# Kernel tuning notes

Measured on AMD Instinct MI355X. Metric: run time of the kernel, lower is better.

Reference implementation:

```python
import jax, jax.numpy as jnp
import numpy as np

B, T, C, H, D = 4, 2048, 1024, 16, 64
EPS = 1e-5

def setup_inputs() -> dict:
    key = jax.random.key(0)
    ks = jax.random.split(key, 8)
    s = lambda fan_in: 1.0 / np.sqrt(fan_in)
    return {
        'x': jax.random.normal(ks[0], (B, T, C), jnp.float32),
        'wq': jax.random.normal(ks[1], (H, C, D), jnp.float32) * s(C),
        'wk': jax.random.normal(ks[2], (H, C, D), jnp.float32) * s(C),
        'wv': jax.random.normal(ks[3], (H, C, D), jnp.float32) * s(C),
        'w_proj': jax.random.normal(ks[4], (C, C), jnp.float32) * s(C),
        'b_proj': jnp.zeros((C,), jnp.float32),
        'w1': jax.random.normal(ks[5], (C, 4 * C), jnp.float32) * s(C),
        'b1': jnp.zeros((4 * C,), jnp.float32),
        'w2': jax.random.normal(ks[6], (4 * C, C), jnp.float32) * s(4 * C),
        'b2': jnp.zeros((C,), jnp.float32),
        'g1': jnp.ones((C,), jnp.float32),
        'be1': jnp.zeros((C,), jnp.float32),
        'g2': jnp.ones((C,), jnp.float32),
        'be2': jnp.zeros((C,), jnp.float32),
    }

def layer_norm(x, g, b):
    mu = jnp.mean(x, axis=-1, keepdims=True)
    var = jnp.mean(jnp.square(x - mu), axis=-1, keepdims=True)
    return (x - mu) * jax.lax.rsqrt(var + EPS) * g + b

def reference(x, wq, wk, wv, w_proj, b_proj, w1, b1, w2, b2, g1, be1, g2, be2):
    # --- attention (pre-LN) ---
    xn = layer_norm(x, g1, be1)
    q = jnp.einsum('btc,hcd->bhtd', xn, wq)
    k = jnp.einsum('btc,hcd->bhtd', xn, wk)
    v = jnp.einsum('btc,hcd->bhtd', xn, wv)
    # NOTE: original scales by full embedding dim C (not head size)
    scores = jnp.einsum('bhtd,bhsd->bhts', q, k) * (C ** -0.5)
    causal = jnp.tril(jnp.ones((T, T), bool))
    scores = jnp.where(causal, scores, -jnp.inf)
    wei = jax.nn.softmax(scores, axis=-1)
    attn = jnp.einsum('bhts,bhsd->bhtd', wei, v)
    attn = attn.transpose(0, 2, 1, 3).reshape(B, T, C)  # concat heads
    x = x + attn @ w_proj + b_proj
    # --- FFN (pre-LN) ---
    xn2 = layer_norm(x, g2, be2)
    h = jax.nn.relu(xn2 @ w1 + b1)
    x = x + h @ w2 + b2
    return x
```

## Files before the change

### kernel.cpp

```cpp
#include <hip/hip_runtime.h>
#include <hip/hip_bf16.h>

#define B_ 4
#define T_ 2048
#define C_ 1024
#define H_ 16
#define D_ 64
#define M_ (B_*T_)

typedef unsigned short ushort;
typedef __attribute__((ext_vector_type(8))) short short8;
typedef __attribute__((ext_vector_type(8))) unsigned short ushort8;
typedef __attribute__((ext_vector_type(4))) float floatx4;
typedef __attribute__((ext_vector_type(4))) unsigned int uintx4;

static __device__ __forceinline__ float bf2f(ushort u) {
    unsigned int x = ((unsigned int)u) << 16;
    return __builtin_bit_cast(float, x);
}
static __device__ __forceinline__ ushort f2bf(float f) {
    unsigned int x = __builtin_bit_cast(unsigned int, f);
    unsigned int r = (x + 0x7fffu + ((x >> 16) & 1u)) >> 16;
    return (ushort)r;
}

typedef const __attribute__((address_space(1))) unsigned int gu32;
typedef __attribute__((address_space(3))) unsigned int lu32;
static __device__ __forceinline__ void glds16(const void* g, void* l) {
    __builtin_amdgcn_global_load_lds((gu32*)g, (lu32*)l, 16, 0, 0);
}

__global__ __launch_bounds__(256) void ln_kernel(
    const float* __restrict__ x, const float* __restrict__ g,
    const float* __restrict__ be, ushort* __restrict__ out)
{
    int row = blockIdx.x;
    int tid = threadIdx.x;
    const float* xr = x + (size_t)row * C_;
    float v[4];
    float s = 0.f, s2 = 0.f;
#pragma unroll
    for (int i = 0; i < 4; i++) {
        float t = xr[tid + i * 256];
        v[i] = t; s += t; s2 += t * t;
    }
#pragma unroll
    for (int off = 32; off; off >>= 1) {
        s  += __shfl_down(s, off);
        s2 += __shfl_down(s2, off);
    }
    __shared__ float rs[4], rs2[4];
    __shared__ float smu, srstd;
    int w = tid >> 6;
    if ((tid & 63) == 0) { rs[w] = s; rs2[w] = s2; }
    __syncthreads();
    if (tid == 0) {
        float ts  = rs[0] + rs[1] + rs[2] + rs[3];
        float ts2 = rs2[0] + rs2[1] + rs2[2] + rs2[3];
        float mu  = ts * (1.f / C_);
        float var = ts2 * (1.f / C_) - mu * mu;
        smu = mu; srstd = rsqrtf(var + 1e-5f);
    }
    __syncthreads();
    float mu = smu, r = srstd;
#pragma unroll
    for (int i = 0; i < 4; i++) {
        int c = tid + i * 256;
        out[(size_t)row * C_ + c] = f2bf((v[i] - mu) * r * g[c] + be[c]);
    }
}

__global__ __launch_bounds__(256) void transpose_conv(
    const float* __restrict__ in, ushort* __restrict__ out,
    int R, int Cn, long long in_bstride, long long out_bstride)
{
    __shared__ float tile[32][33];
    const float* ip = in + (size_t)blockIdx.z * in_bstride;
    ushort* op = out + (size_t)blockIdx.z * out_bstride;
    int tx = threadIdx.x;
    int ty = threadIdx.y;
    int c0 = blockIdx.x * 32, r0 = blockIdx.y * 32;
#pragma unroll
    for (int i = 0; i < 32; i += 8) {
        tile[ty + i][tx] = ip[(size_t)(r0 + ty + i) * Cn + c0 + tx];
    }
    __syncthreads();
#pragma unroll
    for (int i = 0; i < 32; i += 8) {
        int oc = c0 + ty + i;
        int orr = r0 + tx;
        op[(size_t)oc * R + orr] = f2bf(tile[tx][ty + i]);
    }
}

__global__ __launch_bounds__(256) void vtrans_kernel(
    const ushort* __restrict__ qkv, ushort* __restrict__ VtG)
{
    int bh = blockIdx.y;
    int b = bh >> 4, h = bh & 15;
    int j0 = blockIdx.x * 64;
    int tid = threadIdx.x;
    __shared__ unsigned int X[64 * 33];
    const ushort* Vg = qkv + (size_t)(b * T_) * 3072 + 2048 + h * 64;
#pragma unroll
    for (int it = 0; it < 2; it++) {
        int j = (tid >> 3) + it * 32;
        int dp = (tid & 7) * 4;
        uintx4 val = *(const uintx4*)(Vg + (size_t)(j0 + j) * 3072 + dp * 2);
#pragma unroll
        for (int k = 0; k < 4; k++) X[j * 33 + dp + k] = val[k];
    }
    __syncthreads();
    int dp = tid >> 3, jc = tid & 7;
    unsigned int v[8];
#pragma unroll
    for (int jj = 0; jj < 8; jj++) v[jj] = X[(jc * 8 + jj) * 33 + dp];
    ushort8 lo, hi;
#pragma unroll
    for (int jj = 0; jj < 8; jj++) {
        lo[jj] = (ushort)(v[jj] & 0xffffu);
        hi[jj] = (ushort)(v[jj] >> 16);
    }
    size_t r0 = ((size_t)(h * 256 + 4 * (2 * dp) + b)) * T_ + j0 + jc * 8;
    size_t r1 = ((size_t)(h * 256 + 4 * (2 * dp + 1) + b)) * T_ + j0 + jc * 8;
    *(ushort8*)&VtG[r0] = lo;
    *(ushort8*)&VtG[r1] = hi;
}

template<bool OUTBF16, bool BIAS, bool RELU, bool RESID>
__global__ __launch_bounds__(256, 2) void gemm_kernel(
    const ushort* __restrict__ A,
    const ushort* __restrict__ Bt,
    const float* __restrict__ bias,
    const float* __restrict__ resid,
    void* __restrict__ Cout,
    int Mdim, int Ndim, int K)
{
    __shared__ ushort As[128 * 64];
    __shared__ ushort Bs[128 * 64];
    int m0 = blockIdx.y * 128, n0 = blockIdx.x * 128;
    int tid = threadIdx.x;
    int wave = tid >> 6, lane = tid & 63;
    int quad = lane >> 4, l16 = lane & 15;
    int wm = (wave >> 1) * 64, wn = (wave & 1) * 64;
    floatx4 acc[4][4] = {};

    int lrow = lane >> 3;
    int lchunk = (lane & 7) ^ (lrow & 7);

    for (int k0 = 0; k0 < K; k0 += 64) {
        __syncthreads();
#pragma unroll
        for (int it = 0; it < 4; it++) {
            int rb = wave * 32 + it * 8;
            int r  = rb + lrow;
            glds16(A  + (size_t)(m0 + r) * K + k0 + lchunk * 8, &As[rb * 64]);
            glds16(Bt + (size_t)(n0 + r) * K + k0 + lchunk * 8, &Bs[rb * 64]);
        }
        __syncthreads();
#pragma unroll
        for (int kk = 0; kk < 2; kk++) {
            short8 af[4], bfv[4];
            int c = kk * 4 + quad;
            int sw = (c ^ (l16 & 7)) * 8;
#pragma unroll
            for (int mi = 0; mi < 4; mi++)
                af[mi] = *(const short8*)&As[(wm + mi * 16 + l16) * 64 + sw];
#pragma unroll
            for (int ni = 0; ni < 4; ni++)
                bfv[ni] = *(const short8*)&Bs[(wn + ni * 16 + l16) * 64 + sw];
#pragma unroll
            for (int mi = 0; mi < 4; mi++)
#pragma unroll
                for (int ni = 0; ni < 4; ni++)
                    acc[mi][ni] = __builtin_amdgcn_mfma_f32_16x16x32_bf16(af[mi], bfv[ni], acc[mi][ni], 0, 0, 0);
        }
    }

    int r4 = quad * 4;
#pragma unroll
    for (int mi = 0; mi < 4; mi++) {
#pragma unroll
        for (int ni = 0; ni < 4; ni++) {
#pragma unroll
            for (int r = 0; r < 4; r++) {
                int gm = m0 + wm + mi * 16 + r4 + r;
                int gn = n0 + wn + ni * 16 + l16;
                float v = acc[mi][ni][r];
                if (BIAS)  v += bias[gn];
                if (RESID) v += resid[(size_t)gm * Ndim + gn];
                if (RELU)  v = fmaxf(v, 0.f);
                if (OUTBF16) ((ushort*)Cout)[(size_t)gm * Ndim + gn] = f2bf(v);
                else         ((float*)Cout)[(size_t)gm * Ndim + gn] = v;
            }
        }
    }
}

__global__ __launch_bounds__(256, 2) void attn_kernel(
    const ushort* __restrict__ qkv,
    const ushort* __restrict__ VtG,
    ushort* __restrict__ attnb)
{
    const int LD = 3072;
    int bid = blockIdx.x;
    int bh = (bid & 7) * 8 + ((bid >> 3) & 7);
    int qt = 15 - (bid >> 6);
    int b = bh >> 4, h = bh & 15;
    int t0 = qt * 128;
    int tid = threadIdx.x;
    int wave = tid >> 6, lane = tid & 63;
    int quad = lane >> 4, l16 = lane & 15;

    __shared__ ushort Ks[2][64 * 64];
    __shared__ ushort Vt[2][64 * 64];
    __shared__ ushort Ps[4][32 * 72];

    const ushort* Qg = qkv + (size_t)(b * T_) * LD + h * 64;
    const ushort* Kg = Qg + 1024;
    const ushort* VtB = VtG + (size_t)(h * 256 + b) * T_;

    int qrow_base = t0 + wave * 32;
    int lrow = lane >> 3;
    int lchunk = (lane & 7) ^ (lrow & 7);

    short8 qa[2][2];
#pragma unroll
    for (int mt = 0; mt < 2; mt++) {
        const ushort* qp = Qg + (size_t)(qrow_base + mt * 16 + l16) * LD + quad * 8;
        ushort8 q0 = *(const ushort8*)qp;
        ushort8 q1 = *(const ushort8*)(qp + 32);
        ushort8 a0, a1;
#pragma unroll
        for (int d = 0; d < 8; d++) {
            a0[d] = f2bf(bf2f(q0[d]) * 0.03125f);
            a1[d] = f2bf(bf2f(q1[d]) * 0.03125f);
        }
        qa[mt][0] = __builtin_bit_cast(short8, a0);
        qa[mt][1] = __builtin_bit_cast(short8, a1);
    }

    float l_part[2][4];
    floatx4 o_acc[2][4];
#pragma unroll
    for (int mt = 0; mt < 2; mt++)
#pragma unroll
        for (int r = 0; r < 4; r++) {
            l_part[mt][r] = 0.f;
            o_acc[mt][r] = floatx4{0.f, 0.f, 0.f, 0.f};
        }

    int nIter = t0 / 64 + 2;

#pragma unroll
    for (int it = 0; it < 2; it++) {
        int rb = (wave * 2 + it) * 8;
        int r = rb + lrow;
        glds16(Kg  + (size_t)r * LD + lchunk * 8, &Ks[0][rb * 64]);
        glds16(VtB + (size_t)r * (4 * T_) + lchunk * 8, &Vt[0][rb * 64]);
    }

    for (int ii = 0; ii < nIter; ii++) {
        int s0 = ii * 64;
        int buf = ii & 1;
        __syncthreads();
        if (ii + 1 < nIter) {
            int sn = s0 + 64;
#pragma unroll
            for (int it = 0; it < 2; it++) {
                int rb = (wave * 2 + it) * 8;
                int r = rb + lrow;
                glds16(Kg  + (size_t)(sn + r) * LD + lchunk * 8, &Ks[buf ^ 1][rb * 64]);
                glds16(VtB + (size_t)r * (4 * T_) + sn + lchunk * 8, &Vt[buf ^ 1][rb * 64]);
            }
        }

        if (s0 <= qrow_base + 31) {
#pragma unroll
            for (int mt = 0; mt < 2; mt++) {
                floatx4 s_acc[4];
#pragma unroll
                for (int nt = 0; nt < 4; nt++) {
                    int krow = nt * 16 + l16;
                    const short8* kb0 = (const short8*)&Ks[buf][krow * 64 + ((quad       ^ (l16 & 7)) * 8)];
                    const short8* kb1 = (const short8*)&Ks[buf][krow * 64 + (((4 + quad) ^ (l16 & 7)) * 8)];
                    floatx4 z = {0.f, 0.f, 0.f, 0.f};
                    z = __builtin_amdgcn_mfma_f32_16x16x32_bf16(qa[mt][0], *kb0, z, 0, 0, 0);
                    s_acc[nt] = __builtin_amdgcn_mfma_f32_16x16x32_bf16(qa[mt][1], *kb1, z, 0, 0, 0);
                }
                int base_mt = qrow_base + mt * 16;
                if (s0 + 63 > base_mt) {
#pragma unroll
                    for (int nt = 0; nt < 4; nt++)
#pragma unroll
                        for (int r = 0; r < 4; r++) {
                            int gi = base_mt + quad * 4 + r;
                            int gj = s0 + nt * 16 + l16;
                            if (gj > gi) s_acc[nt][r] = -INFINITY;
                        }
                }
#pragma unroll
                for (int nt = 0; nt < 4; nt++)
#pragma unroll
                    for (int r = 0; r < 4; r++) {
                        float e = __expf(s_acc[nt][r]);
                        s_acc[nt][r] = e;
                        l_part[mt][r] += e;
                        Ps[wave][(mt * 16 + quad * 4 + r) * 72 + nt * 16 + l16] = f2bf(e);
                    }
            }
            asm volatile("s_waitcnt lgkmcnt(0)" ::: "memory");
            short8 pa[2][2];
#pragma unroll
            for (int mt = 0; mt < 2; mt++) {
                pa[mt][0] = *(const short8*)&Ps[wave][(mt * 16 + l16) * 72 + quad * 8];
                pa[mt][1] = *(const short8*)&Ps[wave][(mt * 16 + l16) * 72 + quad * 8 + 32];
            }
#pragma unroll
            for (int dt = 0; dt < 4; dt++) {
                int vrow = dt * 16 + l16;
                const short8* vb0 = (const short8*)&Vt[buf][vrow * 64 + ((quad       ^ (l16 & 7)) * 8)];
                const short8* vb1 = (const short8*)&Vt[buf][vrow * 64 + (((4 + quad) ^ (l16 & 7)) * 8)];
#pragma unroll
                for (int mt = 0; mt < 2; mt++) {
                    o_acc[mt][dt] = __builtin_amdgcn_mfma_f32_16x16x32_bf16(pa[mt][0], *vb0, o_acc[mt][dt], 0, 0, 0);
                    o_acc[mt][dt] = __builtin_amdgcn_mfma_f32_16x16x32_bf16(pa[mt][1], *vb1, o_acc[mt][dt], 0, 0, 0);
                }
            }
        }
    }

#pragma unroll
    for (int mt = 0; mt < 2; mt++)
#pragma unroll
        for (int r = 0; r < 4; r++) {
            float ls = l_part[mt][r];
            ls += __shfl_xor(ls, 1);
            ls += __shfl_xor(ls, 2);
            ls += __shfl_xor(ls, 4);
            ls += __shfl_xor(ls, 8);
            float inv = 1.f / ls;
            int gi = qrow_base + mt * 16 + quad * 4 + r;
            ushort* op = attnb + (size_t)(b * T_ + gi) * 1024 + h * 64;
#pragma unroll
            for (int dt = 0; dt < 4; dt++)
                op[dt * 16 + l16] = f2bf(o_acc[mt][dt][r] * inv);
        }
}

extern "C" void kernel_launch(void* const* d_in, const int* in_sizes, int n_in,
                              void* d_out, int out_size, void* d_ws, size_t ws_size,
                              hipStream_t stream) {
    (void)in_sizes; (void)n_in; (void)out_size; (void)ws_size;
    const float* x      = (const float*)d_in[0];
    const float* wq     = (const float*)d_in[1];
    const float* wk     = (const float*)d_in[2];
    const float* wv     = (const float*)d_in[3];
    const float* w_proj = (const float*)d_in[4];
    const float* b_proj = (const float*)d_in[5];
    const float* w1     = (const float*)d_in[6];
    const float* b1     = (const float*)d_in[7];
    const float* w2     = (const float*)d_in[8];
    const float* b2     = (const float*)d_in[9];
    const float* g1     = (const float*)d_in[10];
    const float* be1    = (const float*)d_in[11];
    const float* g2     = (const float*)d_in[12];
    const float* be2    = (const float*)d_in[13];
    float* out = (float*)d_out;

    char* ws = (char*)d_ws;
    const size_t MB = 1024ull * 1024ull;
    ushort* xn     = (ushort*)(ws + 0);
    ushort* qkv    = (ushort*)(ws + 16 * MB);
    ushort* attnb  = (ushort*)(ws + 64 * MB);
    ushort* hbuf   = (ushort*)(ws + 16 * MB);
    float*  x1     = (float*) (ws + 80 * MB);
    ushort* VtG    = (ushort*)(ws + 80 * MB);
    ushort* WqkvT  = (ushort*)(ws + 112 * MB);
    ushort* WprojT = (ushort*)(ws + 118 * MB);
    ushort* W1T    = (ushort*)(ws + 120 * MB);
    ushort* W2T    = (ushort*)(ws + 128 * MB);
    ushort* xn2 = xn;

    dim3 tb(32, 8);
    ln_kernel<<<M_, 256, 0, stream>>>(x, g1, be1, xn);
    transpose_conv<<<dim3(D_ / 32, C_ / 32, H_), tb, 0, stream>>>(wq, WqkvT,               C_, D_, (long long)C_ * D_, (long long)D_ * C_);
    transpose_conv<<<dim3(D_ / 32, C_ / 32, H_), tb, 0, stream>>>(wk, WqkvT + C_ * C_,     C_, D_, (long long)C_ * D_, (long long)D_ * C_);
    transpose_conv<<<dim3(D_ / 32, C_ / 32, H_), tb, 0, stream>>>(wv, WqkvT + 2 * C_ * C_, C_, D_, (long long)C_ * D_, (long long)D_ * C_);
    transpose_conv<<<dim3(C_ / 32, C_ / 32, 1), tb, 0, stream>>>(w_proj, WprojT, C_, C_, 0, 0);
    transpose_conv<<<dim3(4 * C_ / 32, C_ / 32, 1), tb, 0, stream>>>(w1, W1T, C_, 4 * C_, 0, 0);
    transpose_conv<<<dim3(C_ / 32, 4 * C_ / 32, 1), tb, 0, stream>>>(w2, W2T, 4 * C_, C_, 0, 0);
    gemm_kernel<true, false, false, false><<<dim3(3072 / 128, M_ / 128), 256, 0, stream>>>(
        xn, WqkvT, nullptr, nullptr, qkv, M_, 3072, C_);
    vtrans_kernel<<<dim3(T_ / 64, B_ * H_), 256, 0, stream>>>(qkv, VtG);
    attn_kernel<<<1024, 256, 0, stream>>>(qkv, VtG, attnb);
    gemm_kernel<false, true, false, true><<<dim3(C_ / 128, M_ / 128), 256, 0, stream>>>(
        attnb, WprojT, b_proj, x, x1, M_, C_, C_);
    ln_kernel<<<M_, 256, 0, stream>>>(x1, g2, be2, xn2);
    gemm_kernel<true, true, true, false><<<dim3(4 * C_ / 128, M_ / 128), 256, 0, stream>>>(
        xn2, W1T, b1, nullptr, hbuf, M_, 4 * C_, C_);
    gemm_kernel<false, true, false, true><<<dim3(C_ / 128, M_ / 128), 256, 0, stream>>>(
        hbuf, W2T, b2, x1, out, M_, C_, 4 * C_);
}
```

Baseline: 455.0 us.

## Double-buffer GEMM LDS tiles and remap blocks for XCD-local L2 reuse

The GEMM kernel now keeps two LDS buffers for the A and B tiles and prefetches the next K-slice with global-to-LDS loads while the MFMAs run on the current one, removing one barrier per iteration. The grid becomes 1D, with block IDs remapped so each of the 8 XCDs works on a contiguous band of 8 M-tiles across all N-tiles, aiming to improve L2 reuse of A rows. LDS use per block doubles to 64KB, which may limit occupancy to two blocks per CU. The mapping hardcodes 64 M-tiles, matching M=8192.

New measurement: 471.0 us. +3.5%, slower.

```diff
diff --git a/kernel.cpp b/kernel.cpp
--- a/kernel.cpp
+++ b/kernel.cpp
@@ -134,11 +134,16 @@
     const float* __restrict__ bias,
     const float* __restrict__ resid,
     void* __restrict__ Cout,
-    int Mdim, int Ndim, int K)
+    int Ndim, int K, int Nt)
 {
-    __shared__ ushort As[128 * 64];
-    __shared__ ushort Bs[128 * 64];
-    int m0 = blockIdx.y * 128, n0 = blockIdx.x * 128;
+    __shared__ ushort As[2][128 * 64];
+    __shared__ ushort Bs[2][128 * 64];
+    int bid = blockIdx.x;
+    int xcd = bid & 7;
+    int loc = bid >> 3;
+    int m0 = (xcd * 8 + loc / Nt) * 128;
+    int n0 = (loc % Nt) * 128;
+
     int tid = threadIdx.x;
     int wave = tid >> 6, lane = tid & 63;
     int quad = lane >> 4, l16 = lane & 15;
@@ -147,17 +152,31 @@
 
     int lrow = lane >> 3;
     int lchunk = (lane & 7) ^ (lrow & 7);
-
-    for (int k0 = 0; k0 < K; k0 += 64) {
+    const ushort* Ab = A  + (size_t)m0 * K + lchunk * 8;
+    const ushort* Bb = Bt + (size_t)n0 * K + lchunk * 8;
+
+    int nK = K >> 6;
+#pragma unroll
+    for (int it = 0; it < 4; it++) {
+        int rb = wave * 32 + it * 8;
+        int r  = rb + lrow;
+        glds16(Ab + (size_t)r * K, &As[0][rb * 64]);
+        glds16(Bb + (size_t)r * K, &Bs[0][rb * 64]);
+    }
+
+    for (int ki = 0; ki < nK; ki++) {
+        int buf = ki & 1;
         __syncthreads();
-#pragma unroll
-        for (int it = 0; it < 4; it++) {
-            int rb = wave * 32 + it * 8;
-            int r  = rb + lrow;
-            glds16(A  + (size_t)(m0 + r) * K + k0 + lchunk * 8, &As[rb * 64]);
-            glds16(Bt + (size_t)(n0 + r) * K + k0 + lchunk * 8, &Bs[rb * 64]);
-        }
-        __syncthreads();
+        if (ki + 1 < nK) {
+            int kn = (ki + 1) * 64;
+#pragma unroll
+            for (int it = 0; it < 4; it++) {
+                int rb = wave * 32 + it * 8;
+                int r  = rb + lrow;
+                glds16(Ab + (size_t)r * K + kn, &As[buf ^ 1][rb * 64]);
+                glds16(Bb + (size_t)r * K + kn, &Bs[buf ^ 1][rb * 64]);
+            }
+        }
 #pragma unroll
         for (int kk = 0; kk < 2; kk++) {
             short8 af[4], bfv[4];
@@ -165,10 +184,10 @@
             int sw = (c ^ (l16 & 7)) * 8;
 #pragma unroll
             for (int mi = 0; mi < 4; mi++)
-                af[mi] = *(const short8*)&As[(wm + mi * 16 + l16) * 64 + sw];
+                af[mi] = *(const short8*)&As[buf][(wm + mi * 16 + l16) * 64 + sw];
 #pragma unroll
             for (int ni = 0; ni < 4; ni++)
-                bfv[ni] = *(const short8*)&Bs[(wn + ni * 16 + l16) * 64 + sw];
+                bfv[ni] = *(const short8*)&Bs[buf][(wn + ni * 16 + l16) * 64 + sw];
 #pragma unroll
             for (int mi = 0; mi < 4; mi++)
 #pragma unroll
@@ -390,15 +409,15 @@
     transpose_conv<<<dim3(C_ / 32, C_ / 32, 1), tb, 0, stream>>>(w_proj, WprojT, C_, C_, 0, 0);
     transpose_conv<<<dim3(4 * C_ / 32, C_ / 32, 1), tb, 0, stream>>>(w1, W1T, C_, 4 * C_, 0, 0);
     transpose_conv<<<dim3(C_ / 32, 4 * C_ / 32, 1), tb, 0, stream>>>(w2, W2T, 4 * C_, C_, 0, 0);
-    gemm_kernel<true, false, false, false><<<dim3(3072 / 128, M_ / 128), 256, 0, stream>>>(
-        xn, WqkvT, nullptr, nullptr, qkv, M_, 3072, C_);
+    gemm_kernel<true, false, false, false><<<64 * 24, 256, 0, stream>>>(
+        xn, WqkvT, nullptr, nullptr, qkv, 3072, C_, 24);
     vtrans_kernel<<<dim3(T_ / 64, B_ * H_), 256, 0, stream>>>(qkv, VtG);
     attn_kernel<<<1024, 256, 0, stream>>>(qkv, VtG, attnb);
-    gemm_kernel<false, true, false, true><<<dim3(C_ / 128, M_ / 128), 256, 0, stream>>>(
-        attnb, WprojT, b_proj, x, x1, M_, C_, C_);
+    gemm_kernel<false, true, false, true><<<64 * 8, 256, 0, stream>>>(
+        attnb, WprojT, b_proj, x, x1, C_, C_, 8);
     ln_kernel<<<M_, 256, 0, stream>>>(x1, g2, be2, xn2);
-    gemm_kernel<true, true, true, false><<<dim3(4 * C_ / 128, M_ / 128), 256, 0, stream>>>(
-        xn2, W1T, b1, nullptr, hbuf, M_, 4 * C_, C_);
-    gemm_kernel<false, true, false, true><<<dim3(C_ / 128, M_ / 128), 256, 0, stream>>>(
-        hbuf, W2T, b2, x1, out, M_, C_, 4 * C_);
-}
+    gemm_kernel<true, true, true, false><<<64 * 32, 256, 0, stream>>>(
+        xn2, W1T, b1, nullptr, hbuf, 4 * C_, C_, 32);
+    gemm_kernel<false, true, false, true><<<64 * 8, 256, 0, stream>>>(
+        hbuf, W2T, b2, x1, out, C_, 4 * C_, 8);
+}
```
